# Kernel optimization log

Measured on AMD Instinct MI355X. Metric: run time of the kernel, lower is better.

## Reference

```python
import jax, jax.numpy as jnp
import numpy as np

N_NODES = 25000
N_EDGES = 50000
NODE_DIM = 64
EDGE_DIM = 16
HIDDEN_DIM = 128


def setup_inputs() -> dict:
    key = jax.random.key(0)
    ks = jax.random.split(key, 12)
    s = 0.05  # small init scale for params
    return {
        "x": jax.random.normal(ks[0], (N_NODES, NODE_DIM), dtype=jnp.float32),
        "edge_index": jax.random.randint(ks[1], (2, N_EDGES), 0, N_NODES, dtype=jnp.int64),
        "edge_attr": jax.random.normal(ks[2], (N_EDGES, EDGE_DIM), dtype=jnp.float32),
        "W1": jax.random.normal(ks[3], (HIDDEN_DIM, EDGE_DIM), dtype=jnp.float32) * s,
        "b1": jax.random.normal(ks[4], (HIDDEN_DIM,), dtype=jnp.float32) * s,
        "W2": jax.random.normal(ks[5], (NODE_DIM * NODE_DIM, HIDDEN_DIM), dtype=jnp.float32) * s,
        "b2": jax.random.normal(ks[6], (NODE_DIM * NODE_DIM,), dtype=jnp.float32) * s,
        "w_ih": jax.random.normal(ks[7], (3 * NODE_DIM, NODE_DIM), dtype=jnp.float32) * s,
        "w_hh": jax.random.normal(ks[8], (3 * NODE_DIM, NODE_DIM), dtype=jnp.float32) * s,
        "b_ih": jax.random.normal(ks[9], (3 * NODE_DIM,), dtype=jnp.float32) * s,
        "b_hh": jax.random.normal(ks[10], (3 * NODE_DIM,), dtype=jnp.float32) * s,
    }


def reference(x, edge_index, edge_attr, W1, b1, W2, b2, w_ih, w_hh, b_ih, b_hh):
    n_nodes, d = x.shape
    src, dst = edge_index[0], edge_index[1]
    # edge-conditioned weight matrices: MLP_edge(e_ij) -> (E, d, d)
    h = jax.nn.gelu(edge_attr @ W1.T + b1, approximate=False)
    edge_w = (h @ W2.T + b2).reshape(-1, d, d)
    # per-edge message: W_e @ x_src  (gather + batched matvec)
    messages = jnp.einsum('eij,ej->ei', edge_w, x[src])
    # scatter-add into destination nodes
    agg = jax.ops.segment_sum(messages, dst, num_segments=n_nodes)
    # GRUCell(agg, x): input=agg, hidden=x  (PyTorch gate layout r,z,n)
    gi = agg @ w_ih.T + b_ih
    gh = x @ w_hh.T + b_hh
    i_r, i_z, i_n = jnp.split(gi, 3, axis=-1)
    h_r, h_z, h_n = jnp.split(gh, 3, axis=-1)
    r = jax.nn.sigmoid(i_r + h_r)
    z = jax.nn.sigmoid(i_z + h_z)
    n = jnp.tanh(i_n + r * h_n)
    return (1.0 - z) * n + z * x
```

## Files before the change

### kernel.cpp

```cpp
#include <hip/hip_runtime.h>
#include <math.h>


constexpr int N_NODES  = 25000;
constexpr int N_EDGES  = 50000;
constexpr int NODE_DIM = 64;
constexpr int EDGE_DIM = 16;
constexpr int HID      = 128;

typedef __attribute__((ext_vector_type(8))) _Float16 half8;
typedef __attribute__((ext_vector_type(4))) float    f32x4;

constexpr int G_MS  = 128;
constexpr int G_PK  = 270;
constexpr int G_MLP = N_EDGES / 8;

__global__ __launch_bounds__(256) void prep_kernel(
    const float* __restrict__ W2, const float* __restrict__ b2,
    const float* __restrict__ w_ih, const float* __restrict__ w_hh,
    const float* __restrict__ edge_attr, const float* __restrict__ W1,
    const float* __restrict__ b1,
    _Float16* __restrict__ Wpk, _Float16* __restrict__ b2pk,
    _Float16* __restrict__ gpk,
    _Float16* __restrict__ h, float* __restrict__ agg)
{
    int b = blockIdx.x;
    if (b < G_MS) {
        float4* a4 = (float4*)agg;
        const float4 z = make_float4(0.f, 0.f, 0.f, 0.f);
        for (int i = b * 256 + threadIdx.x; i < N_NODES * NODE_DIM / 4; i += G_MS * 256)
            a4[i] = z;
        return;
    }
    if (b < G_MS + G_PK) {
        int c = (b - G_MS) * 256 + threadIdx.x;
        if (c < 65536) {
            int lane = c & 63, mt = (c >> 6) & 3, ks = (c >> 8) & 3, j = c >> 10;
            int i   = mt * 16 + (lane & 15);
            int col = ks * 32 + ((lane >> 4) & 3) * 8;
            const float* src = W2 + (size_t)(i * 64 + j) * HID + col;
            half8 o;
#pragma unroll
            for (int q = 0; q < 8; ++q) o[q] = (_Float16)src[q];
            ((half8*)Wpk)[c] = o;
        } else if (c < 65536 + 512) {
            int c2 = c - 65536;
            int lane = c2 & 63, mt = (c2 >> 6) & 3, ks2 = (c2 >> 8) & 1;
            int i = mt * 16 + (lane & 15);
            int j = ks2 * 32 + ((lane >> 4) & 3) * 8;
            const float* src = b2 + i * 64 + j;
            half8 o;
#pragma unroll
            for (int q = 0; q < 8; ++q) o[q] = (_Float16)src[q];
            ((half8*)b2pk)[c2] = o;
        } else if (c < 65536 + 512 + 3072) {
            int c3 = c - (65536 + 512);
            int lane = c3 & 63, ks = (c3 >> 6) & 1;
            int t2 = c3 >> 7;
            int nt = t2 % 12, mat = t2 / 12;
            int g = nt * 16 + (lane & 15);
            int k = ks * 32 + ((lane >> 4) & 3) * 8;
            const float* src = (mat == 0 ? w_ih : w_hh) + (size_t)g * 64 + k;
            half8 o;
#pragma unroll
            for (int q = 0; q < 8; ++q) o[q] = (_Float16)src[q];
            ((half8*)gpk)[c3] = o;
        }
        return;
    }
    int ebase = (b - G_MS - G_PK) * 8;
    int k = threadIdx.x & 127;
    const float* w = W1 + (size_t)k * EDGE_DIM;
#pragma unroll
    for (int p = 0; p < 4; ++p) {
        int e = ebase + p * 2 + (threadIdx.x >> 7);
        if (e >= N_EDGES) break;
        const float* ea = edge_attr + (size_t)e * EDGE_DIM;
        float acc = b1[k];
#pragma unroll
        for (int d = 0; d < EDGE_DIM; ++d) acc += ea[d] * w[d];
        float g = 0.5f * acc * (1.0f + erff(acc * 0.70710678118654752f));
        h[(size_t)e * HID + k] = (_Float16)g;
    }
}

__global__ __launch_bounds__(256, 3) void edge_msg_mfma_kernel(
    const _Float16* __restrict__ hbuf,
    const float*    __restrict__ x,
    const int*      __restrict__ edge_index,
    const _Float16* __restrict__ Wpk,
    const _Float16* __restrict__ b2pk,
    float* __restrict__ agg)
{
    __shared__ float xsh[64 * 68];
    __shared__ float msgred[64 * 67];
    __shared__ int   dsts[64];

    const int e0   = blockIdx.x * 64;
    const int t    = threadIdx.x;
    const int mt   = t >> 6;
    const int lane = t & 63;

    {
        int le = t >> 2, sub = t & 3;
        int e = e0 + le;
        int s = -1;
        if (e < N_EDGES) {
            if (sub == 0) dsts[le] = edge_index[N_EDGES + e];
            s = edge_index[e];
        } else if (sub == 0) {
            dsts[le] = -1;
        }
#pragma unroll
        for (int q = 0; q < 4; ++q) {
            float4 v = make_float4(0.f, 0.f, 0.f, 0.f);
            if ((unsigned)s < (unsigned)N_NODES)
                v = ((const float4*)x)[(size_t)s * 16 + sub * 4 + q];
            *(float4*)&xsh[le * 68 + sub * 16 + q * 4] = v;
        }
    }

    half8 hf[4][4];
#pragma unroll
    for (int nt = 0; nt < 4; ++nt) {
#pragma unroll
        for (int ks = 0; ks < 4; ++ks) {
            int el = nt * 16 + (lane & 15);
            int ee = e0 + el; if (ee >= N_EDGES) ee = N_EDGES - 1;
            int gk = ks * 32 + ((lane >> 4) & 3) * 8;
            hf[nt][ks] = *(const half8*)(hbuf + (size_t)ee * HID + gk);
        }
    }
    __syncthreads();

    const f32x4 zero4 = {0.f, 0.f, 0.f, 0.f};
    f32x4 msg[4];
#pragma unroll
    for (int nt = 0; nt < 4; ++nt) msg[nt] = zero4;

    const half8* wpk8 = (const half8*)Wpk;
    const int mbase = mt * 64 + lane;

    half8 aA[4], aB[4];
#pragma unroll
    for (int ks = 0; ks < 4; ++ks) aA[ks] = wpk8[(size_t)mbase + ks * 256];

#pragma unroll 1
    for (int j = 0; j < 64; j += 2) {
        {
            size_t nb = (size_t)(j + 1) * 1024 + mbase;
#pragma unroll
            for (int ks = 0; ks < 4; ++ks) aB[ks] = wpk8[nb + ks * 256];
        }
        {
            float gv[4];
#pragma unroll
            for (int nt = 0; nt < 4; ++nt) gv[nt] = xsh[(nt * 16 + (lane & 15)) * 68 + j];
            f32x4 P[4];
#pragma unroll
            for (int ks = 0; ks < 4; ++ks)
#pragma unroll
                for (int nt = 0; nt < 4; ++nt)
                    P[nt] = __builtin_amdgcn_mfma_f32_16x16x32_f16(
                        aA[ks], hf[nt][ks], ks == 0 ? zero4 : P[nt], 0, 0, 0);
#pragma unroll
            for (int nt = 0; nt < 4; ++nt)
#pragma unroll
                for (int r = 0; r < 4; ++r) msg[nt][r] += gv[nt] * P[nt][r];
        }
        if (j + 2 < 64) {
            size_t nb = (size_t)(j + 2) * 1024 + mbase;
#pragma unroll
            for (int ks = 0; ks < 4; ++ks) aA[ks] = wpk8[nb + ks * 256];
        }
        {
            float gv[4];
#pragma unroll
            for (int nt = 0; nt < 4; ++nt) gv[nt] = xsh[(nt * 16 + (lane & 15)) * 68 + j + 1];
            f32x4 P[4];
#pragma unroll
            for (int ks = 0; ks < 4; ++ks)
#pragma unroll
                for (int nt = 0; nt < 4; ++nt)
                    P[nt] = __builtin_amdgcn_mfma_f32_16x16x32_f16(
                        aB[ks], hf[nt][ks], ks == 0 ? zero4 : P[nt], 0, 0, 0);
#pragma unroll
            for (int nt = 0; nt < 4; ++nt)
#pragma unroll
                for (int r = 0; r < 4; ++r) msg[nt][r] += gv[nt] * P[nt][r];
        }
    }

#pragma unroll
    for (int ks2 = 0; ks2 < 2; ++ks2) {
        half8 gf[4];
#pragma unroll
        for (int nt = 0; nt < 4; ++nt) {
            const float* gp = &xsh[(nt * 16 + (lane & 15)) * 68 + ks2 * 32 + ((lane >> 4) & 3) * 8];
            float4 lo = *(const float4*)gp;
            float4 hi = *(const float4*)(gp + 4);
            half8 g8;
            g8[0] = (_Float16)lo.x; g8[1] = (_Float16)lo.y;
            g8[2] = (_Float16)lo.z; g8[3] = (_Float16)lo.w;
            g8[4] = (_Float16)hi.x; g8[5] = (_Float16)hi.y;
            g8[6] = (_Float16)hi.z; g8[7] = (_Float16)hi.w;
            gf[nt] = g8;
        }
        half8 bf8 = ((const half8*)b2pk)[ks2 * 256 + mt * 64 + lane];
#pragma unroll
        for (int nt = 0; nt < 4; ++nt)
            msg[nt] = __builtin_amdgcn_mfma_f32_16x16x32_f16(bf8, gf[nt], msg[nt], 0, 0, 0);
    }

#pragma unroll
    for (int nt = 0; nt < 4; ++nt)
#pragma unroll
        for (int r = 0; r < 4; ++r) {
            int i = mt * 16 + ((lane >> 4) & 3) * 4 + r;
            int e = nt * 16 + (lane & 15);
            msgred[i * 67 + e] = msg[nt][r];
        }
    __syncthreads();

#pragma unroll 1
    for (int ee = mt; ee < 64; ee += 4) {
        int d = dsts[ee];
        if (e0 + ee < N_EDGES && (unsigned)d < (unsigned)N_NODES)
            atomicAdd(agg + (size_t)d * NODE_DIM + lane, msgred[lane * 67 + ee]);
    }
}

__global__ __launch_bounds__(256) void gru_mfma_kernel(
    const float* __restrict__ agg,
    const float* __restrict__ x,
    const _Float16* __restrict__ gpk,
    const float* __restrict__ b_ih,
    const float* __restrict__ b_hh,
    float* __restrict__ out)
{
    const int t = threadIdx.x, wave = t >> 6, lane = t & 63;
    const int n0 = blockIdx.x * 64;

    int arow = n0 + wave * 16 + (lane & 15);
    if (arow >= N_NODES) arow = N_NODES - 1;
    const int kcol = ((lane >> 4) & 3) * 8;
    half8 aF[2], xF[2];
#pragma unroll
    for (int ks = 0; ks < 2; ++ks) {
        const float* ap = agg + (size_t)arow * 64 + ks * 32 + kcol;
        const float* xp = x   + (size_t)arow * 64 + ks * 32 + kcol;
        float4 a0 = *(const float4*)ap, a1 = *(const float4*)(ap + 4);
        float4 x0 = *(const float4*)xp, x1 = *(const float4*)(xp + 4);
        half8 af, xf;
        af[0] = (_Float16)a0.x; af[1] = (_Float16)a0.y; af[2] = (_Float16)a0.z; af[3] = (_Float16)a0.w;
        af[4] = (_Float16)a1.x; af[5] = (_Float16)a1.y; af[6] = (_Float16)a1.z; af[7] = (_Float16)a1.w;
        xf[0] = (_Float16)x0.x; xf[1] = (_Float16)x0.y; xf[2] = (_Float16)x0.z; xf[3] = (_Float16)x0.w;
        xf[4] = (_Float16)x1.x; xf[5] = (_Float16)x1.y; xf[6] = (_Float16)x1.z; xf[7] = (_Float16)x1.w;
        aF[ks] = af; xF[ks] = xf;
    }

    const half8* g8 = (const half8*)gpk;
    const f32x4 zero4 = {0.f, 0.f, 0.f, 0.f};
    f32x4 accI[12], accH[12];
#pragma unroll
    for (int nt = 0; nt < 12; ++nt) {
        half8 b0 = g8[((0 * 12 + nt) * 2 + 0) * 64 + lane];
        half8 b1 = g8[((0 * 12 + nt) * 2 + 1) * 64 + lane];
        f32x4 a = __builtin_amdgcn_mfma_f32_16x16x32_f16(aF[0], b0, zero4, 0, 0, 0);
        accI[nt] = __builtin_amdgcn_mfma_f32_16x16x32_f16(aF[1], b1, a, 0, 0, 0);
        half8 c0 = g8[((1 * 12 + nt) * 2 + 0) * 64 + lane];
        half8 c1 = g8[((1 * 12 + nt) * 2 + 1) * 64 + lane];
        f32x4 h0 = __builtin_amdgcn_mfma_f32_16x16x32_f16(xF[0], c0, zero4, 0, 0, 0);
        accH[nt] = __builtin_amdgcn_mfma_f32_16x16x32_f16(xF[1], c1, h0, 0, 0, 0);
    }

    const int nodeBase = n0 + wave * 16 + ((lane >> 4) & 3) * 4;
    const int dlo = lane & 15;
#pragma unroll
    for (int q = 0; q < 4; ++q) {
        int d = q * 16 + dlo;
        float bi0 = b_ih[d], bi1 = b_ih[64 + d], bi2 = b_ih[128 + d];
        float bh0 = b_hh[d], bh1 = b_hh[64 + d], bh2 = b_hh[128 + d];
#pragma unroll
        for (int r = 0; r < 4; ++r) {
            int node = nodeBase + r;
            if (node < N_NODES) {
                float I0 = accI[q][r] + bi0, I1 = accI[q + 4][r] + bi1, I2 = accI[q + 8][r] + bi2;
                float H0 = accH[q][r] + bh0, H1 = accH[q + 4][r] + bh1, H2 = accH[q + 8][r] + bh2;
                float rg = 1.f / (1.f + expf(-(I0 + H0)));
                float z  = 1.f / (1.f + expf(-(I1 + H1)));
                float nn = tanhf(I2 + rg * H2);
                float xv = x[(size_t)node * 64 + d];
                out[(size_t)node * 64 + d] = (1.f - z) * nn + z * xv;
            }
        }
    }
}

extern "C" void kernel_launch(void* const* d_in, const int* in_sizes, int n_in,
                              void* d_out, int out_size, void* d_ws, size_t ws_size,
                              hipStream_t stream)
{
    const float* x          = (const float*)d_in[0];
    const int*   edge_index = (const int*)  d_in[1];
    const float* edge_attr  = (const float*)d_in[2];
    const float* W1         = (const float*)d_in[3];
    const float* b1         = (const float*)d_in[4];
    const float* W2         = (const float*)d_in[5];
    const float* b2         = (const float*)d_in[6];
    const float* w_ih       = (const float*)d_in[7];
    const float* w_hh       = (const float*)d_in[8];
    const float* b_ih       = (const float*)d_in[9];
    const float* b_hh       = (const float*)d_in[10];
    float* out = (float*)d_out;

    char* ws = (char*)d_ws;
    _Float16* hbuf = (_Float16*)ws;
    ws += (size_t)N_EDGES * HID * sizeof(_Float16);
    _Float16* Wpk  = (_Float16*)ws;
    ws += (size_t)65536 * 8 * sizeof(_Float16);
    _Float16* b2pk = (_Float16*)ws;
    ws += (size_t)512 * 8 * sizeof(_Float16);
    _Float16* gpk  = (_Float16*)ws;
    ws += (size_t)64 * 192 * sizeof(float);
    ws += (size_t)64 * 192 * sizeof(float);
    float* agg = (float*)ws;

    prep_kernel<<<dim3(G_MS + G_PK + G_MLP), dim3(256), 0, stream>>>(
        W2, b2, w_ih, w_hh, edge_attr, W1, b1,
        Wpk, b2pk, gpk, hbuf, agg);

    edge_msg_mfma_kernel<<<dim3((N_EDGES + 63) / 64), dim3(256), 0, stream>>>(
        hbuf, x, edge_index, Wpk, b2pk, agg);

    gru_mfma_kernel<<<dim3((N_NODES + 63) / 64), dim3(256), 0, stream>>>(
        agg, x, gpk, b_ih, b_hh, out);
}
```

Measured before the change: 107.4 us.

## Fuse edge MLP first layer and GELU into the edge message kernel

Computes the per-edge hidden activations (edge_attr·W1ᵀ + b1, then exact GELU) inside the edge message kernel and stages them in shared memory, reusing the msgred buffer. Previously prep_kernel ran 6250 extra blocks that wrote a 50000×128 fp16 buffer to global memory, which the message kernel then read back. Removing that round trip and those blocks is meant to cut HBM traffic and launch work. The cost is extra shared memory for W1/b1, two more barriers, and per-thread ALU work that may affect occupancy in the MFMA kernel.

New measurement: 100.4 us. -6.5%, faster.

```diff
diff --git a/kernel.cpp b/kernel.cpp
--- a/kernel.cpp
+++ b/kernel.cpp
@@ -13,16 +13,12 @@
 
 constexpr int G_MS  = 128;
 constexpr int G_PK  = 270;
-constexpr int G_MLP = N_EDGES / 8;
 
 __global__ __launch_bounds__(256) void prep_kernel(
     const float* __restrict__ W2, const float* __restrict__ b2,
     const float* __restrict__ w_ih, const float* __restrict__ w_hh,
-    const float* __restrict__ edge_attr, const float* __restrict__ W1,
-    const float* __restrict__ b1,
     _Float16* __restrict__ Wpk, _Float16* __restrict__ b2pk,
-    _Float16* __restrict__ gpk,
-    _Float16* __restrict__ h, float* __restrict__ agg)
+    _Float16* __restrict__ gpk, float* __restrict__ agg)
 {
     int b = blockIdx.x;
     if (b < G_MS) {
@@ -32,60 +28,45 @@
             a4[i] = z;
         return;
     }
-    if (b < G_MS + G_PK) {
-        int c = (b - G_MS) * 256 + threadIdx.x;
-        if (c < 65536) {
-            int lane = c & 63, mt = (c >> 6) & 3, ks = (c >> 8) & 3, j = c >> 10;
-            int i   = mt * 16 + (lane & 15);
-            int col = ks * 32 + ((lane >> 4) & 3) * 8;
-            const float* src = W2 + (size_t)(i * 64 + j) * HID + col;
-            half8 o;
-#pragma unroll
-            for (int q = 0; q < 8; ++q) o[q] = (_Float16)src[q];
-            ((half8*)Wpk)[c] = o;
-        } else if (c < 65536 + 512) {
-            int c2 = c - 65536;
-            int lane = c2 & 63, mt = (c2 >> 6) & 3, ks2 = (c2 >> 8) & 1;
-            int i = mt * 16 + (lane & 15);
-            int j = ks2 * 32 + ((lane >> 4) & 3) * 8;
-            const float* src = b2 + i * 64 + j;
-            half8 o;
-#pragma unroll
-            for (int q = 0; q < 8; ++q) o[q] = (_Float16)src[q];
-            ((half8*)b2pk)[c2] = o;
-        } else if (c < 65536 + 512 + 3072) {
-            int c3 = c - (65536 + 512);
-            int lane = c3 & 63, ks = (c3 >> 6) & 1;
-            int t2 = c3 >> 7;
-            int nt = t2 % 12, mat = t2 / 12;
-            int g = nt * 16 + (lane & 15);
-            int k = ks * 32 + ((lane >> 4) & 3) * 8;
-            const float* src = (mat == 0 ? w_ih : w_hh) + (size_t)g * 64 + k;
-            half8 o;
-#pragma unroll
-            for (int q = 0; q < 8; ++q) o[q] = (_Float16)src[q];
-            ((half8*)gpk)[c3] = o;
-        }
-        return;
-    }
-    int ebase = (b - G_MS - G_PK) * 8;
-    int k = threadIdx.x & 127;
-    const float* w = W1 + (size_t)k * EDGE_DIM;
-#pragma unroll
-    for (int p = 0; p < 4; ++p) {
-        int e = ebase + p * 2 + (threadIdx.x >> 7);
-        if (e >= N_EDGES) break;
-        const float* ea = edge_attr + (size_t)e * EDGE_DIM;
-        float acc = b1[k];
-#pragma unroll
-        for (int d = 0; d < EDGE_DIM; ++d) acc += ea[d] * w[d];
-        float g = 0.5f * acc * (1.0f + erff(acc * 0.70710678118654752f));
-        h[(size_t)e * HID + k] = (_Float16)g;
+    int c = (b - G_MS) * 256 + threadIdx.x;
+    if (c < 65536) {
+        int lane = c & 63, mt = (c >> 6) & 3, ks = (c >> 8) & 3, j = c >> 10;
+        int i   = mt * 16 + (lane & 15);
+        int col = ks * 32 + ((lane >> 4) & 3) * 8;
+        const float* src = W2 + (size_t)(i * 64 + j) * HID + col;
+        half8 o;
+#pragma unroll
+        for (int q = 0; q < 8; ++q) o[q] = (_Float16)src[q];
+        ((half8*)Wpk)[c] = o;
+    } else if (c < 65536 + 512) {
+        int c2 = c - 65536;
+        int lane = c2 & 63, mt = (c2 >> 6) & 3, ks2 = (c2 >> 8) & 1;
+        int i = mt * 16 + (lane & 15);
+        int j = ks2 * 32 + ((lane >> 4) & 3) * 8;
+        const float* src = b2 + i * 64 + j;
+        half8 o;
+#pragma unroll
+        for (int q = 0; q < 8; ++q) o[q] = (_Float16)src[q];
+        ((half8*)b2pk)[c2] = o;
+    } else if (c < 65536 + 512 + 3072) {
+        int c3 = c - (65536 + 512);
+        int lane = c3 & 63, ks = (c3 >> 6) & 1;
+        int t2 = c3 >> 7;
+        int nt = t2 % 12, mat = t2 / 12;
+        int g = nt * 16 + (lane & 15);
+        int k = ks * 32 + ((lane >> 4) & 3) * 8;
+        const float* src = (mat == 0 ? w_ih : w_hh) + (size_t)g * 64 + k;
+        half8 o;
+#pragma unroll
+        for (int q = 0; q < 8; ++q) o[q] = (_Float16)src[q];
+        ((half8*)gpk)[c3] = o;
     }
 }
 
 __global__ __launch_bounds__(256, 3) void edge_msg_mfma_kernel(
-    const _Float16* __restrict__ hbuf,
+    const float*    __restrict__ edge_attr,
+    const float*    __restrict__ W1,
+    const float*    __restrict__ b1,
     const float*    __restrict__ x,
     const int*      __restrict__ edge_index,
     const _Float16* __restrict__ Wpk,
@@ -94,7 +75,10 @@
 {
     __shared__ float xsh[64 * 68];
     __shared__ float msgred[64 * 67];
+    __shared__ float W1s[128 * 16];
+    __shared__ float b1s[128];
     __shared__ int   dsts[64];
+    _Float16* hsh = (_Float16*)msgred;
 
     const int e0   = blockIdx.x * 64;
     const int t    = threadIdx.x;
@@ -120,15 +104,52 @@
         }
     }
 
+#pragma unroll
+    for (int r = 0; r < 8; ++r) W1s[t + r * 256] = W1[t + r * 256];
+    if (t < 128) b1s[t] = b1[t];
+    __syncthreads();
+
+    {
+        int le = t >> 2, sub = t & 3;
+        int e = e0 + le;
+        float ea[16];
+        if (e < N_EDGES) {
+            const float4* ea4 = (const float4*)(edge_attr + (size_t)e * EDGE_DIM);
+#pragma unroll
+            for (int q = 0; q < 4; ++q) {
+                float4 v = ea4[q];
+                ea[q * 4] = v.x; ea[q * 4 + 1] = v.y; ea[q * 4 + 2] = v.z; ea[q * 4 + 3] = v.w;
+            }
+        } else {
+#pragma unroll
+            for (int d = 0; d < 16; ++d) ea[d] = 0.f;
+        }
+#pragma unroll
+        for (int kc = 0; kc < 4; ++kc) {
+            half8 hh;
+#pragma unroll
+            for (int kk = 0; kk < 8; ++kk) {
+                int k = sub * 32 + kc * 8 + kk;
+                float acc = b1s[k];
+                const float* w = &W1s[k * 16];
+#pragma unroll
+                for (int d = 0; d < EDGE_DIM; ++d) acc += ea[d] * w[d];
+                float g = 0.5f * acc * (1.0f + erff(acc * 0.70710678118654752f));
+                hh[kk] = (_Float16)g;
+            }
+            *(half8*)&hsh[le * 128 + sub * 32 + kc * 8] = hh;
+        }
+    }
+    __syncthreads();
+
     half8 hf[4][4];
 #pragma unroll
     for (int nt = 0; nt < 4; ++nt) {
 #pragma unroll
         for (int ks = 0; ks < 4; ++ks) {
             int el = nt * 16 + (lane & 15);
-            int ee = e0 + el; if (ee >= N_EDGES) ee = N_EDGES - 1;
             int gk = ks * 32 + ((lane >> 4) & 3) * 8;
-            hf[nt][ks] = *(const half8*)(hbuf + (size_t)ee * HID + gk);
+            hf[nt][ks] = *(const half8*)&hsh[el * 128 + gk];
         }
     }
     __syncthreads();
@@ -265,9 +286,9 @@
 #pragma unroll
     for (int nt = 0; nt < 12; ++nt) {
         half8 b0 = g8[((0 * 12 + nt) * 2 + 0) * 64 + lane];
-        half8 b1 = g8[((0 * 12 + nt) * 2 + 1) * 64 + lane];
+        half8 b1f = g8[((0 * 12 + nt) * 2 + 1) * 64 + lane];
         f32x4 a = __builtin_amdgcn_mfma_f32_16x16x32_f16(aF[0], b0, zero4, 0, 0, 0);
-        accI[nt] = __builtin_amdgcn_mfma_f32_16x16x32_f16(aF[1], b1, a, 0, 0, 0);
+        accI[nt] = __builtin_amdgcn_mfma_f32_16x16x32_f16(aF[1], b1f, a, 0, 0, 0);
         half8 c0 = g8[((1 * 12 + nt) * 2 + 0) * 64 + lane];
         half8 c1 = g8[((1 * 12 + nt) * 2 + 1) * 64 + lane];
         f32x4 h0 = __builtin_amdgcn_mfma_f32_16x16x32_f16(xF[0], c0, zero4, 0, 0, 0);
@@ -315,7 +336,6 @@
     float* out = (float*)d_out;
 
     char* ws = (char*)d_ws;
-    _Float16* hbuf = (_Float16*)ws;
     ws += (size_t)N_EDGES * HID * sizeof(_Float16);
     _Float16* Wpk  = (_Float16*)ws;
     ws += (size_t)65536 * 8 * sizeof(_Float16);
@@ -326,12 +346,11 @@
     ws += (size_t)64 * 192 * sizeof(float);
     float* agg = (float*)ws;
 
-    prep_kernel<<<dim3(G_MS + G_PK + G_MLP), dim3(256), 0, stream>>>(
-        W2, b2, w_ih, w_hh, edge_attr, W1, b1,
-        Wpk, b2pk, gpk, hbuf, agg);
+    prep_kernel<<<dim3(G_MS + G_PK), dim3(256), 0, stream>>>(
+        W2, b2, w_ih, w_hh, Wpk, b2pk, gpk, agg);
 
     edge_msg_mfma_kernel<<<dim3((N_EDGES + 63) / 64), dim3(256), 0, stream>>>(
-        hbuf, x, edge_index, Wpk, b2pk, agg);
+        edge_attr, W1, b1, x, edge_index, Wpk, b2pk, agg);
 
     gru_mfma_kernel<<<dim3((N_NODES + 63) / 64), dim3(256), 0, stream>>>(
         agg, x, gpk, b_ih, b_hh, out);
```
